# Performance work log

Measured on AMD Instinct MI355X. Metric: run time of the kernel, lower is better.

Reference implementation:

```python
import jax, jax.numpy as jnp
import numpy as np

NUM_HEADS = 16

def setup_inputs() -> dict:
    key = jax.random.key(0)
    k1, k2, k3, k4 = jax.random.split(key, 4)
    B, N, C = 4, 2048, 1024
    x = jax.random.normal(k1, (B, N, C), dtype=jnp.float32)
    xpos = jax.random.randint(k2, (B, N), 0, 2048, dtype=jnp.int64)
    Wqkv = jax.random.normal(k3, (C, 3 * C), dtype=jnp.float32) * (C ** -0.5)
    Wproj = jax.random.normal(k4, (C, C), dtype=jnp.float32) * (C ** -0.5)
    bproj = jnp.zeros((C,), dtype=jnp.float32)
    return {"x": x, "xpos": xpos, "Wqkv": Wqkv, "Wproj": Wproj, "bproj": bproj}

def reference(x, xpos, Wqkv, Wproj, bproj):
    # rope is None in this configuration, so xpos is unused (matches torch default path).
    B, N, C = x.shape
    H = NUM_HEADS
    Dh = C // H
    scale = Dh ** -0.5
    qkv = jnp.einsum('bnc,cd->bnd', x, Wqkv)              # [B, N, 3C]
    qkv = qkv.reshape(B, N, 3, H, Dh)
    q, k, v = qkv[:, :, 0], qkv[:, :, 1], qkv[:, :, 2]    # [B, N, H, Dh]
    scores = jnp.einsum('bnhd,bmhd->bhnm', q, k) * scale  # [B, H, N, N]
    attn = jax.nn.softmax(scores, axis=-1)
    out = jnp.einsum('bhnm,bmhd->bnhd', attn, v)          # [B, N, H, Dh]
    out = out.reshape(B, N, C)
    return jnp.einsum('bnc,cd->bnd', out, Wproj) + bproj
```

## Files before the change

kernel.cpp:

```cpp
#include <hip/hip_runtime.h>
#include <stdint.h>

#define DEVINL __device__ __forceinline__

typedef __bf16 bf16x8 __attribute__((ext_vector_type(8)));
typedef float f32x4 __attribute__((ext_vector_type(4)));
typedef float f32x16 __attribute__((ext_vector_type(16)));
typedef uint32_t u32x4 __attribute__((ext_vector_type(4)));

DEVINL uint16_t f2bf(float f) {
    uint32_t u = __builtin_bit_cast(uint32_t, f);
    uint32_t r = (u + 0x7FFFu + ((u >> 16) & 1u)) >> 16;
    return (uint16_t)r;
}

DEVINL bf16x8 ld8(const uint16_t* p) {
    u32x4 v = *(const u32x4*)p;
    return __builtin_bit_cast(bf16x8, v);
}

DEVINL void gload16(const void* g, void* l) {
    __builtin_amdgcn_global_load_lds(
        (const __attribute__((address_space(1))) uint32_t*)g,
        (__attribute__((address_space(3))) uint32_t*)l, 16, 0, 0);
}

DEVINL uint32_t cvtpk(float lo, float hi) {
    uint32_t r;
    asm("v_cvt_pk_bf16_f32 %0, %1, %2" : "=v"(r) : "v"(lo), "v"(hi));
    return r;
}

DEVINL float exp2_fast(float x) {
    float r;
    asm("v_exp_f32 %0, %1" : "=v"(r) : "v"(x));
    return r;
}

DEVINL void transW_body(const float* __restrict__ W, uint16_t* __restrict__ WT,
                        int Nn, int n0, int k0, int tid, uint16_t* t) {
#pragma unroll
    for (int i = 0; i < 4; ++i) {
        int c = tid + i * 256;
        int kr = c >> 4, nc = c & 15;
        float4 v = *(const float4*)(W + (size_t)(k0 + kr) * Nn + n0 + nc * 4);
        t[(nc * 4 + 0) * 65 + kr] = f2bf(v.x);
        t[(nc * 4 + 1) * 65 + kr] = f2bf(v.y);
        t[(nc * 4 + 2) * 65 + kr] = f2bf(v.z);
        t[(nc * 4 + 3) * 65 + kr] = f2bf(v.w);
    }
    __syncthreads();
#pragma unroll
    for (int i = 0; i < 2; ++i) {
        int c = tid + i * 256;
        int nr = c >> 3, kc = c & 7;
        union { uint16_t u[8]; u32x4 v; } o;
#pragma unroll
        for (int j = 0; j < 8; ++j) o.u[j] = t[nr * 65 + kc * 8 + j];
        *(u32x4*)(WT + (size_t)(n0 + nr) * 1024 + k0 + kc * 8) = o.v;
    }
}

__global__ void k_prep(const float* __restrict__ x, uint16_t* __restrict__ xb,
                       const float* __restrict__ Wqkv, uint16_t* __restrict__ wqkvT,
                       const float* __restrict__ Wproj, uint16_t* __restrict__ wprojT) {
    __shared__ uint16_t t[64 * 65];
    int bid = blockIdx.x;
    int tid = threadIdx.x;
    if (bid < 4096) {
        int i = bid * 256 + tid;
        const float4* src = (const float4*)x + (size_t)i * 2;
        float4 a = src[0], b = src[1];
        union { uint16_t u[8]; u32x4 v; } o;
        o.u[0] = f2bf(a.x); o.u[1] = f2bf(a.y); o.u[2] = f2bf(a.z); o.u[3] = f2bf(a.w);
        o.u[4] = f2bf(b.x); o.u[5] = f2bf(b.y); o.u[6] = f2bf(b.z); o.u[7] = f2bf(b.w);
        ((u32x4*)xb)[i] = o.v;
    } else if (bid < 4864) {
        int idx = bid - 4096;
        transW_body(Wqkv, wqkvT, 3072, (idx % 48) * 64, (idx / 48) * 64, tid, t);
    } else {
        int idx = bid - 4864;
        transW_body(Wproj, wprojT, 1024, (idx % 16) * 64, (idx / 16) * 64, tid, t);
    }
}

template <int MODE>
__global__ __launch_bounds__(512) void k_gemm(
    const uint16_t* __restrict__ A, const uint16_t* __restrict__ BT,
    const float* __restrict__ bias,
    uint16_t* __restrict__ qo, uint16_t* __restrict__ ko, uint16_t* __restrict__ vo,
    float* __restrict__ out) {
    extern __shared__ uint16_t lds[];
    int tid = threadIdx.x;
    int w = tid >> 6, l = tid & 63;
    int l15 = l & 15, l4 = l >> 4;
    int wr = w >> 2, wc = w & 3;
    int bid = blockIdx.x;
    int mt = (bid & 7) * 4 + ((bid >> 3) & 3);
    int nt = bid >> 5;
    int m0 = mt * 256, n0 = nt * 128;

    int r0 = tid >> 3, sl0 = tid & 7;
    int kc = sl0 ^ (r0 & 7);
    const uint16_t* pA = A + (size_t)(m0 + r0) * 1024 + kc * 8;
    const uint16_t* pB = BT + (size_t)(n0 + r0) * 1024 + kc * 8;
    int wofs = w * 512;

    f32x4 acc[8][2] = {};

    auto stageA = [&](int ks, int abA) {
#pragma unroll
        for (int q = 0; q < 4; ++q)
            gload16(pA + q * 65536 + ks * 64, lds + abA + q * 4096 + wofs);
    };
    auto stageB = [&](int ks, int abB) {
#pragma unroll
        for (int li = 0; li < 2; ++li)
            gload16(pB + li * 65536 + ks * 64, lds + abB + li * 4096 + wofs);
    };

    auto computeHalf = [&](int abA, int abB, int kk) {
        const uint16_t* Ah = lds + abA + wr * 8192;
        const uint16_t* Bb = lds + abB;
        int ch = ((kk * 4 + l4) ^ (l15 & 7)) * 8;
        bf16x8 af[8], bf[2];
#pragma unroll
        for (int fi = 0; fi < 8; ++fi)
            af[fi] = ld8(Ah + (fi * 16 + l15) * 64 + ch);
#pragma unroll
        for (int fj = 0; fj < 2; ++fj)
            bf[fj] = ld8(Bb + (wc * 32 + fj * 16 + l15) * 64 + ch);
        __builtin_amdgcn_s_setprio(1);
#pragma unroll
        for (int fi = 0; fi < 8; ++fi)
#pragma unroll
            for (int fj = 0; fj < 2; ++fj)
                acc[fi][fj] = __builtin_amdgcn_mfma_f32_16x16x32_bf16(
                    af[fi], bf[fj], acc[fi][fj], 0, 0, 0);
        __builtin_amdgcn_s_setprio(0);
    };

    auto step = [&](int s, int abA, int abB, int abAn, int abBn) {
        bool pf = (s + 1 < 16);
        if (pf) stageA(s + 1, abAn);
        computeHalf(abA, abB, 0);
        if (pf) stageB(s + 1, abBn);
        computeHalf(abA, abB, 1);
        asm volatile("s_waitcnt vmcnt(0)\n\ts_barrier" ::: "memory");
    };

    stageA(0, 0); stageB(0, 32768);
    asm volatile("s_waitcnt vmcnt(0)\n\ts_barrier" ::: "memory");
    for (int s = 0; s < 16; s += 2) {
        step(s,     0,     32768, 16384, 40960);
        step(s + 1, 16384, 40960, 0,     32768);
    }

    if constexpr (MODE == 0) {
        int b = m0 >> 11, nbase = m0 & 2047;
        if (n0 >= 2048) {
#pragma unroll
            for (int fi = 0; fi < 8; ++fi)
#pragma unroll
                for (int fj = 0; fj < 2; ++fj) {
                    int dl = wc * 32 + fj * 16 + l15;
                    int ml = wr * 128 + fi * 16 + l4 * 4;
                    union { uint16_t u[4]; uint2 v2; } pk;
#pragma unroll
                    for (int r = 0; r < 4; ++r) pk.u[r] = f2bf(acc[fi][fj][r]);
                    *(uint2*)&lds[dl * 264 + ml] = pk.v2;
                }
        __syncthreads();
#pragma unroll
            for (int it = 0; it < 8; ++it) {
                int idx = it * 512 + tid;
                int row = idx >> 5, col = (idx & 31) * 8;
                u32x4 val = *(u32x4*)&lds[row * 264 + col];
                int dv = (n0 - 2048) + row;
                int h = dv >> 6, dh = dv & 63;
                *(u32x4*)(vo + ((size_t)(b * 16 + h) * 64 + dh) * 2048 + nbase + col) = val;
            }
        } else {
            float sc = (n0 < 1024) ? 0.18033688011112042f : 1.0f;
            uint16_t* dst0 = (n0 < 1024) ? qo : ko;
#pragma unroll
            for (int fi = 0; fi < 8; ++fi)
#pragma unroll
                for (int fj = 0; fj < 2; ++fj) {
                    int d = n0 + wc * 32 + fj * 16 + l15;
                    int h = (d >> 6) & 15, dh = d & 63;
#pragma unroll
                    for (int r = 0; r < 4; ++r) {
                        int n = nbase + wr * 128 + fi * 16 + l4 * 4 + r;
                        dst0[((size_t)(b * 16 + h) * 2048 + n) * 64 + dh] = f2bf(acc[fi][fj][r] * sc);
                    }
                }
        }
    } else {
#pragma unroll
        for (int fj = 0; fj < 2; ++fj) {
            int d = n0 + wc * 32 + fj * 16 + l15;
            float bv = bias[d];
#pragma unroll
            for (int fi = 0; fi < 8; ++fi)
#pragma unroll
                for (int r = 0; r < 4; ++r) {
                    int m = m0 + wr * 128 + fi * 16 + l4 * 4 + r;
                    out[(size_t)m * 1024 + d] = acc[fi][fj][r] + bv;
                }
        }
    }
}

__global__ __launch_bounds__(256) void k_attn(
    const uint16_t* __restrict__ q, const uint16_t* __restrict__ kk_,
    const uint16_t* __restrict__ vt, uint16_t* __restrict__ o) {
    __shared__ uint16_t k_lds[2][128 * 64];
    __shared__ uint16_t v_lds[2][64 * 128];
    int tid = threadIdx.x;
    int w = tid >> 6, l = tid & 63;
    int l31 = l & 31, g = l >> 5;
    int bid = blockIdx.x;
    int slot = bid >> 3;
    int bh = (bid & 7) * 8 + (slot >> 4);
    int qt = slot & 15;
    int qrow = qt * 128 + w * 32 + l31;
    const uint16_t* qb = q + ((size_t)bh * 2048 + qrow) * 64;
    const uint16_t* kbase = kk_ + (size_t)bh * 2048 * 64;
    const uint16_t* vbase = vt + (size_t)bh * 64 * 2048;

    bf16x8 qf[4];
#pragma unroll
    for (int kv = 0; kv < 4; ++kv) qf[kv] = ld8(qb + kv * 16 + g * 8);

    int c0 = w * 256 + l;
    int rrK = c0 >> 3, slK = c0 & 7;
    int kcK = slK ^ (rrK & 7);
    const uint16_t* kp = kbase + (size_t)rrK * 64 + kcK * 8;
    int rv0 = w * 16 + (l >> 4);
    int sv = l & 15;
    const uint16_t* vpp0 = vbase + (size_t)(rv0 + 0)  * 2048 + (sv ^ ((rv0 + 0)  & 7)) * 8;
    const uint16_t* vpp1 = vbase + (size_t)(rv0 + 4)  * 2048 + (sv ^ ((rv0 + 4)  & 7)) * 8;
    const uint16_t* vpp2 = vbase + (size_t)(rv0 + 8)  * 2048 + (sv ^ ((rv0 + 8)  & 7)) * 8;
    const uint16_t* vpp3 = vbase + (size_t)(rv0 + 12) * 2048 + (sv ^ ((rv0 + 12) & 7)) * 8;
    uint16_t* kd0 = k_lds[0] + w * 2048;
    uint16_t* kd1 = k_lds[1] + w * 2048;
    uint16_t* vd0 = v_lds[0] + w * 2048;
    uint16_t* vd1 = v_lds[1] + w * 2048;

    f32x16 oa[2] = {};
    float lsum = 0.f;

    auto stage = [&](uint16_t* kd, uint16_t* vd) {
        gload16(kp,        kd);        gload16(kp + 512,  kd + 512);
        gload16(kp + 1024, kd + 1024); gload16(kp + 1536, kd + 1536);
        gload16(vpp0, vd);        gload16(vpp1, vd + 512);
        gload16(vpp2, vd + 1024); gload16(vpp3, vd + 1536);
        kp += 8192;
        vpp0 += 128; vpp1 += 128; vpp2 += 128; vpp3 += 128;
    };

    stage(kd0, vd0);

    auto body = [&](int t, const uint16_t* kb, const uint16_t* vb,
                    uint16_t* kdn, uint16_t* vdn) {
        asm volatile("s_waitcnt vmcnt(4)\n\ts_barrier" ::: "memory");
        if (t < 15) stage(kdn, vdn);

        bf16x8 pfrag[8];
#pragma unroll
        for (int j = 0; j < 4; ++j) {
            int key = j * 32 + l31;
            f32x16 stj = {};
            __builtin_amdgcn_s_setprio(1);
#pragma unroll
            for (int kv = 0; kv < 4; ++kv) {
                bf16x8 kf = ld8(kb + key * 64 + ((2 * kv + g) ^ (key & 7)) * 8);
                stj = __builtin_amdgcn_mfma_f32_32x32x16_bf16(kf, qf[kv], stj, 0, 0, 0);
            }
            __builtin_amdgcn_s_setprio(0);
#pragma unroll
            for (int h = 0; h < 2; ++h) {
                float e[8];
#pragma unroll
                for (int jj = 0; jj < 8; ++jj) e[jj] = exp2_fast(stj[h * 8 + jj]);
                lsum += ((e[0] + e[1]) + (e[2] + e[3])) + ((e[4] + e[5]) + (e[6] + e[7]));
                uint32_t a0 = cvtpk(e[0], e[1]), a1 = cvtpk(e[2], e[3]);
                uint32_t b0 = cvtpk(e[4], e[5]), b1 = cvtpk(e[6], e[7]);
                auto r0 = __builtin_amdgcn_permlane32_swap(a0, b0, false, false);
                auto r1 = __builtin_amdgcn_permlane32_swap(a1, b1, false, false);
                u32x4 f;
                f[0] = r0[0]; f[1] = r1[0]; f[2] = r0[1]; f[3] = r1[1];
                pfrag[j * 2 + h] = __builtin_bit_cast(bf16x8, f);
            }
        }

        if (t < 15) asm volatile("s_waitcnt vmcnt(8)\n\ts_barrier" ::: "memory");
        else        asm volatile("s_waitcnt vmcnt(0)\n\ts_barrier" ::: "memory");

        __builtin_amdgcn_s_setprio(1);
#pragma unroll
        for (int kv = 0; kv < 8; ++kv) {
#pragma unroll
            for (int dt = 0; dt < 2; ++dt) {
                int dh = dt * 32 + l31;
                bf16x8 vf = ld8(vb + dh * 128 + ((2 * kv + g) ^ (dh & 7)) * 8);
                oa[dt] = __builtin_amdgcn_mfma_f32_32x32x16_bf16(vf, pfrag[kv], oa[dt], 0, 0, 0);
            }
        }
        __builtin_amdgcn_s_setprio(0);
    };

    for (int kt = 0; kt < 16; kt += 2) {
        body(kt,     k_lds[0], v_lds[0], kd1, vd1);
        body(kt + 1, k_lds[1], v_lds[1], kd0, vd0);
    }

    float ltot = lsum + __shfl_xor(lsum, 32, 64);
    float inv = 1.0f / ltot;
    int b = bh >> 4, h = bh & 15;
    uint16_t* ob = o + ((size_t)(b * 2048 + qrow)) * 1024 + h * 64;
#pragma unroll
    for (int dt = 0; dt < 2; ++dt)
#pragma unroll
        for (int rq = 0; rq < 4; ++rq) {
            union { uint16_t u[4]; uint2 v; } pk;
#pragma unroll
            for (int rr = 0; rr < 4; ++rr) pk.u[rr] = f2bf(oa[dt][rq * 4 + rr] * inv);
            int dh0 = dt * 32 + rq * 8 + g * 4;
            *(uint2*)(ob + dh0) = pk.v;
        }
}

extern "C" void kernel_launch(void* const* d_in, const int* in_sizes, int n_in,
                              void* d_out, int out_size, void* d_ws, size_t ws_size,
                              hipStream_t stream) {
    const float* x     = (const float*)d_in[0];
    const float* Wqkv  = (const float*)d_in[2];
    const float* Wproj = (const float*)d_in[3];
    const float* bproj = (const float*)d_in[4];
    float* out = (float*)d_out;

    char* ws = (char*)d_ws;
    uint16_t* xb     = (uint16_t*)(ws);
    uint16_t* wqkvT  = (uint16_t*)(ws + 16777216);
    uint16_t* wprojT = (uint16_t*)(ws + 23068672);
    uint16_t* qws    = (uint16_t*)(ws + 25165824);
    uint16_t* kws    = (uint16_t*)(ws + 41943040);
    uint16_t* vT     = (uint16_t*)(ws + 58720256);
    uint16_t* attnout = xb;

    k_prep<<<dim3(5120), dim3(256), 0, stream>>>(x, xb, Wqkv, wqkvT, Wproj, wprojT);
    k_gemm<0><<<dim3(768), dim3(512), 98304, stream>>>(xb, wqkvT, nullptr, qws, kws, vT, nullptr);
    k_attn<<<dim3(1024), dim3(256), 0, stream>>>(qws, kws, vT, attnout);
    k_gemm<1><<<dim3(256), dim3(512), 98304, stream>>>(attnout, wprojT, bproj, nullptr, nullptr, nullptr, out);
}
```

Baseline: 189.1 us.

## Single-buffer V tile in attention kernel, staging V after PV stage

Drops the V tile from double to single buffering, halving V LDS use, and issues the next V load only after the PV MFMAs have consumed the current tile, behind an extra barrier. The PV wait becomes vmcnt(0), which also waits on the K prefetch. The likely intent is a smaller LDS footprint so more blocks fit per CU. In exchange V load latency is no longer hidden across a full iteration, and each step adds a barrier and a full memory wait.

```diff
diff --git a/kernel.cpp b/kernel.cpp
--- a/kernel.cpp
+++ b/kernel.cpp
@@ -216,7 +216,7 @@
     const uint16_t* __restrict__ q, const uint16_t* __restrict__ kk_,
     const uint16_t* __restrict__ vt, uint16_t* __restrict__ o) {
     __shared__ uint16_t k_lds[2][128 * 64];
-    __shared__ uint16_t v_lds[2][64 * 128];
+    __shared__ uint16_t v_lds[64 * 128];
     int tid = threadIdx.x;
     int w = tid >> 6, l = tid & 63;
     int l31 = l & 31, g = l >> 5;
@@ -245,27 +245,28 @@
     const uint16_t* vpp3 = vbase + (size_t)(rv0 + 12) * 2048 + (sv ^ ((rv0 + 12) & 7)) * 8;
     uint16_t* kd0 = k_lds[0] + w * 2048;
     uint16_t* kd1 = k_lds[1] + w * 2048;
-    uint16_t* vd0 = v_lds[0] + w * 2048;
-    uint16_t* vd1 = v_lds[1] + w * 2048;
+    uint16_t* vd  = v_lds + w * 2048;
 
     f32x16 oa[2] = {};
     float lsum = 0.f;
 
-    auto stage = [&](uint16_t* kd, uint16_t* vd) {
+    auto stageK = [&](uint16_t* kd) {
         gload16(kp,        kd);        gload16(kp + 512,  kd + 512);
         gload16(kp + 1024, kd + 1024); gload16(kp + 1536, kd + 1536);
+        kp += 8192;
+    };
+    auto stageV = [&]() {
         gload16(vpp0, vd);        gload16(vpp1, vd + 512);
         gload16(vpp2, vd + 1024); gload16(vpp3, vd + 1536);
-        kp += 8192;
         vpp0 += 128; vpp1 += 128; vpp2 += 128; vpp3 += 128;
     };
 
-    stage(kd0, vd0);
-
-    auto body = [&](int t, const uint16_t* kb, const uint16_t* vb,
-                    uint16_t* kdn, uint16_t* vdn) {
+    stageK(kd0);
+    stageV();
+
+    auto body = [&](int t, const uint16_t* kb, uint16_t* kdn) {
         asm volatile("s_waitcnt vmcnt(4)\n\ts_barrier" ::: "memory");
-        if (t < 15) stage(kdn, vdn);
+        if (t < 15) stageK(kdn);
 
         bf16x8 pfrag[8];
 #pragma unroll
@@ -295,8 +296,7 @@
             }
         }
 
-        if (t < 15) asm volatile("s_waitcnt vmcnt(8)\n\ts_barrier" ::: "memory");
-        else        asm volatile("s_waitcnt vmcnt(0)\n\ts_barrier" ::: "memory");
+        asm volatile("s_waitcnt vmcnt(0)\n\ts_barrier" ::: "memory");
 
         __builtin_amdgcn_s_setprio(1);
 #pragma unroll
@@ -304,16 +304,21 @@
 #pragma unroll
             for (int dt = 0; dt < 2; ++dt) {
                 int dh = dt * 32 + l31;
-                bf16x8 vf = ld8(vb + dh * 128 + ((2 * kv + g) ^ (dh & 7)) * 8);
+                bf16x8 vf = ld8(v_lds + dh * 128 + ((2 * kv + g) ^ (dh & 7)) * 8);
                 oa[dt] = __builtin_amdgcn_mfma_f32_32x32x16_bf16(vf, pfrag[kv], oa[dt], 0, 0, 0);
             }
         }
         __builtin_amdgcn_s_setprio(0);
+
+        if (t < 15) {
+            asm volatile("s_barrier" ::: "memory");
+            stageV();
+        }
     };
 
     for (int kt = 0; kt < 16; kt += 2) {
-        body(kt,     k_lds[0], v_lds[0], kd1, vd1);
-        body(kt + 1, k_lds[1], v_lds[1], kd0, vd0);
+        body(kt,     k_lds[0], kd1);
+        body(kt + 1, k_lds[1], kd0);
     }
 
     float ltot = lsum + __shfl_xor(lsum, 32, 64);
```

New measurement: 231.4 us. 1.22x slower.
